# Kernel optimization log

Hardware: AMD Instinct MI355X
Metric: run time of the kernel (lower is better)

The kernel has to match this reference:

```python
import jax, jax.numpy as jnp
import numpy as np

EPS = 1e-5  # torch BatchNorm1d default eps


def _bn(x, gamma, beta):
    # Training-mode BatchNorm1d: per-batch mean/var (biased), affine.
    mu = jnp.mean(x, axis=0)
    var = jnp.var(x, axis=0)
    return (x - mu) * jax.lax.rsqrt(var + EPS) * gamma + beta


def _trunk(x, layers):
    # For each hidden layer: Tanh(Linear(BatchNorm(x)))
    for (W, b, g, be) in layers:
        x = jnp.tanh(_bn(x, g, be) @ W + b)
    return x


def setup_inputs() -> dict:
    key = jax.random.key(0)
    ks = jax.random.split(key, 16)
    B, N, D = 4096, 8192, 1024
    dims = [D, 1024, 512, 256]
    inp = {
        "x": jax.random.normal(ks[0], (B, D), dtype=jnp.float32),
        "x_n": jax.random.normal(ks[1], (N, D), dtype=jnp.float32),
        "y_n": jax.random.uniform(ks[2], (N, 1), dtype=jnp.float32),
    }
    for i in range(3):
        fan_in, fan_out = dims[i], dims[i + 1]
        bound = 1.0 / np.sqrt(fan_in)
        inp[f"W{i+1}"] = jax.random.uniform(ks[3 + 4 * i], (fan_in, fan_out), minval=-bound, maxval=bound, dtype=jnp.float32)
        inp[f"b{i+1}"] = jax.random.uniform(ks[4 + 4 * i], (fan_out,), minval=-bound, maxval=bound, dtype=jnp.float32)
        inp[f"g{i+1}"] = jnp.ones((fan_in,), dtype=jnp.float32)
        inp[f"beta{i+1}"] = jnp.zeros((fan_in,), dtype=jnp.float32)
    return inp


def reference(x, x_n, y_n,
              W1, b1, g1, beta1,
              W2, b2, g2, beta2,
              W3, b3, g3, beta3):
    layers = [(W1, b1, g1, beta1), (W2, b2, g2, beta2), (W3, b3, g3, beta3)]
    q = _trunk(x, layers)      # [B, 256]
    k = _trunk(x_n, layers)    # [N, 256]
    # l2 similarity: negative squared euclidean distance, via GEMM.
    # sim[i,j] = -||q_i - k_j||^2 = 2 q_i.k_j - ||q_i||^2 - ||k_j||^2
    q2 = jnp.sum(q * q, axis=1, keepdims=True)          # [B,1]
    k2 = jnp.sum(k * k, axis=1)                          # [N]
    sim = 2.0 * (q @ k.T) - q2 - k2[None, :]             # [B,N]
    # x != x_n (different shapes) => train=False, no diagonal masking.
    scores = jax.nn.softmax(sim, axis=1)
    out = jnp.clip(scores @ y_n, 0.0, 1.0)               # [B,1]
    return jnp.squeeze(out, axis=1)                      # [B]
```

## Files before the change

### kernel.cpp

```cpp
#include <hip/hip_runtime.h>
#include <math.h>
#include <stdint.h>


typedef __attribute__((ext_vector_type(8))) _Float16 half8;
typedef __attribute__((ext_vector_type(4))) _Float16 half4;
typedef __attribute__((ext_vector_type(4))) float floatx4;

__device__ __forceinline__ float fast_tanh(float x) {
    float ax = fabsf(x);
    float e  = __expf(-2.0f * ax);
    float r  = (1.0f - e) / (1.0f + e);
    return copysignf(r, x);
}
__device__ __forceinline__ void gload16(const void* g, void* l) {
    __builtin_amdgcn_global_load_lds(
        (__attribute__((address_space(1))) void*)(uintptr_t)(g),
        (__attribute__((address_space(3))) void*)(unsigned int)(uintptr_t)(l),
        16, 0, 0);
}

__global__ __launch_bounds__(256) void tof16_stats_all(
        const float* __restrict__ xn, const float* __restrict__ x,
        _Float16* __restrict__ xnh, _Float16* __restrict__ xh,
        float* __restrict__ cs0, float* __restrict__ cq0,
        float* __restrict__ cs3, float* __restrict__ cq3) {
    const float* in; _Float16* out; float *cs, *cq; int r0;
    if (blockIdx.x < 256) { in = xn; out = xnh; cs = cs0; cq = cq0; r0 = blockIdx.x * 32; }
    else                  { in = x;  out = xh;  cs = cs3; cq = cq3; r0 = (blockIdx.x - 256) * 32; }
    const int c = threadIdx.x * 4;
    float s0 = 0.f, s1 = 0.f, s2 = 0.f, s3 = 0.f;
    float q0 = 0.f, q1 = 0.f, q2 = 0.f, q3 = 0.f;
    for (int r = r0; r < r0 + 32; ++r) {
        float4 v = *(const float4*)&in[(size_t)r * 1024 + c];
        half4 h;
        h[0] = (_Float16)v.x; h[1] = (_Float16)v.y;
        h[2] = (_Float16)v.z; h[3] = (_Float16)v.w;
        *(half4*)&out[(size_t)r * 1024 + c] = h;
        s0 += v.x; q0 += v.x * v.x;
        s1 += v.y; q1 += v.y * v.y;
        s2 += v.z; q2 += v.z * v.z;
        s3 += v.w; q3 += v.w * v.w;
    }
    atomicAdd(&cs[c + 0], s0); atomicAdd(&cq[c + 0], q0);
    atomicAdd(&cs[c + 1], s1); atomicAdd(&cq[c + 1], q1);
    atomicAdd(&cs[c + 2], s2); atomicAdd(&cq[c + 2], q2);
    atomicAdd(&cs[c + 3], s3); atomicAdd(&cq[c + 3], q3);
}

__global__ __launch_bounds__(256) void wprep2(
        const float* __restrict__ W, const float* __restrict__ g,
        const float* __restrict__ beta,
        const float* __restrict__ csK, const float* __restrict__ cqK, float invRK,
        _Float16* __restrict__ WTk, float* __restrict__ baccK,
        const float* __restrict__ csQ, const float* __restrict__ cqQ, float invRQ,
        _Float16* __restrict__ WTq, float* __restrict__ baccQ,
        int C, int F) {
    const int z = blockIdx.z;
    const float* cs = z ? csQ : csK;
    const float* cq = z ? cqQ : cqK;
    const float invR = z ? invRQ : invRK;
    _Float16* WT = z ? WTq : WTk;
    float* bacc = z ? baccQ : baccK;

    __shared__ float sv[32], tv[32];
    __shared__ float tile[32][33];
    __shared__ float lds2[8][32];
    const int c0 = blockIdx.y * 32, f0 = blockIdx.x * 32;
    const int tx = threadIdx.x & 31, ty = threadIdx.x >> 5;
    if (ty == 0) {
        int c = c0 + tx;
        float mean = cs[c] * invR;
        float var  = fmaxf(cq[c] * invR - mean * mean, 0.f);
        float s    = g[c] * rsqrtf(var + 1e-5f);
        sv[tx] = s;
        tv[tx] = beta[c] - mean * s;
    }
    __syncthreads();
    float pacc = 0.f;
#pragma unroll
    for (int i = 0; i < 32; i += 8) {
        float w = W[(size_t)(c0 + ty + i) * F + f0 + tx];
        tile[ty + i][tx] = w * sv[ty + i];
        pacc += w * tv[ty + i];
    }
    lds2[ty][tx] = pacc;
    __syncthreads();
#pragma unroll
    for (int i = 0; i < 32; i += 8)
        WT[(size_t)(f0 + ty + i) * C + c0 + tx] = (_Float16)tile[tx][ty + i];
    if (ty == 0) {
        float a = 0.f;
#pragma unroll
        for (int j = 0; j < 8; ++j) a += lds2[j][tx];
        atomicAdd(&bacc[f0 + tx], a);
    }
}

__global__ __launch_bounds__(256, 2) void gemm_tn_tanh(
        const _Float16* __restrict__ Ak, const _Float16* __restrict__ Aq,
        const _Float16* __restrict__ WTk, const _Float16* __restrict__ WTq,
        const float* __restrict__ bias,
        const float* __restrict__ baccK, const float* __restrict__ baccQ,
        _Float16* __restrict__ Yk, _Float16* __restrict__ Yq,
        int K, int F, int smodeK, int smodeQ,
        float* __restrict__ csK, float* __restrict__ cqK,
        float* __restrict__ csQ, float* __restrict__ cqQ,
        float* __restrict__ rowsqK) {
    __shared__ _Float16 As[128 * 64];
    __shared__ _Float16 Bs[128 * 64];
    const int tid = threadIdx.x;
    const int wv = tid >> 6, ln = tid & 63;
    const int quad = ln >> 4, l16 = ln & 15;
    const int wr = wv >> 1, wc = wv & 1;

    const bool isK = blockIdx.x < 64;
    const _Float16* A  = isK ? Ak : Aq;
    const _Float16* WT = isK ? WTk : WTq;
    const float* bacc  = isK ? baccK : baccQ;
    _Float16* Y        = isK ? Yk : Yq;
    const int smode    = isK ? smodeK : smodeQ;
    float* cs = isK ? csK : csQ;
    float* cq = isK ? cqK : cqQ;
    const int i0 = (isK ? blockIdx.x : blockIdx.x - 64) * 128;
    const int f0 = blockIdx.y * 128;

    floatx4 acc[4][4];
#pragma unroll
    for (int a = 0; a < 4; ++a)
#pragma unroll
        for (int b = 0; b < 4; ++b) acc[a][b] = (floatx4)0.f;

    for (int k0 = 0; k0 < K; k0 += 64) {
        const char* Ab = (const char*)(A + (size_t)i0 * K + k0);
        const char* Bb = (const char*)(WT + (size_t)f0 * K + k0);
#pragma unroll
        for (int it = 0; it < 4; ++it) {
            int seg = it * 256 + tid;
            int row = seg >> 3, p = seg & 7;
            int lcol = (p ^ row) & 7;
            gload16(Ab + (size_t)row * (K * 2) + lcol * 16, (char*)As + seg * 16);
        }
#pragma unroll
        for (int it = 0; it < 4; ++it) {
            int seg = it * 256 + tid;
            int row = seg >> 3, p = seg & 7;
            int lcol = (p ^ row) & 7;
            gload16(Bb + (size_t)row * (K * 2) + lcol * 16, (char*)Bs + seg * 16);
        }
        __syncthreads();
#pragma unroll
        for (int kk = 0; kk < 2; ++kk) {
            half8 af[4], bf[4];
#pragma unroll
            for (int t = 0; t < 4; ++t) {
                int ra = wr * 64 + t * 16 + l16;
                int ca = ((kk * 4 + quad) ^ ra) & 7;
                af[t] = *(const half8*)((const char*)As + ra * 128 + ca * 16);
                int rb = wc * 64 + t * 16 + l16;
                int cb = ((kk * 4 + quad) ^ rb) & 7;
                bf[t] = *(const half8*)((const char*)Bs + rb * 128 + cb * 16);
            }
#pragma unroll
            for (int tr = 0; tr < 4; ++tr)
#pragma unroll
                for (int tc = 0; tc < 4; ++tc)
                    acc[tr][tc] = __builtin_amdgcn_mfma_f32_16x16x32_f16(af[tr], bf[tc], acc[tr][tc], 0, 0, 0);
        }
        __syncthreads();
    }
#pragma unroll
    for (int tc = 0; tc < 4; ++tc) {
        int f = f0 + wc * 64 + tc * 16 + l16;
        float bb = bias[f] + bacc[f];
#pragma unroll
        for (int tr = 0; tr < 4; ++tr)
#pragma unroll
            for (int r = 0; r < 4; ++r) {
                int row = i0 + wr * 64 + tr * 16 + quad * 4 + r;
                float v = fast_tanh(acc[tr][tc][r] + bb);
                acc[tr][tc][r] = v;
                Y[(size_t)row * F + f] = (_Float16)v;
            }
    }
    if (smode == 1) {
#pragma unroll
        for (int tc = 0; tc < 4; ++tc) {
            int f = f0 + wc * 64 + tc * 16 + l16;
            float s = 0.f, q = 0.f;
#pragma unroll
            for (int tr = 0; tr < 4; ++tr)
#pragma unroll
                for (int r = 0; r < 4; ++r) {
                    float v = acc[tr][tc][r];
                    s += v; q += v * v;
                }
            s += __shfl_xor(s, 16); q += __shfl_xor(q, 16);
            s += __shfl_xor(s, 32); q += __shfl_xor(q, 32);
            if (quad == 0) {
                atomicAdd(&cs[f], s);
                atomicAdd(&cq[f], q);
            }
        }
    } else if (smode == 2) {
#pragma unroll
        for (int tr = 0; tr < 4; ++tr)
#pragma unroll
            for (int r = 0; r < 4; ++r) {
                float rq = 0.f;
#pragma unroll
                for (int tc = 0; tc < 4; ++tc) {
                    float v = acc[tr][tc][r];
                    rq += v * v;
                }
                rq += __shfl_xor(rq, 1); rq += __shfl_xor(rq, 2);
                rq += __shfl_xor(rq, 4); rq += __shfl_xor(rq, 8);
                if (l16 == 0)
                    atomicAdd(&rowsqK[i0 + wr * 64 + tr * 16 + quad * 4 + r], rq);
            }
    }
}

__global__ __launch_bounds__(256, 2) void flash_mfma(
        const _Float16* __restrict__ Q, const _Float16* __restrict__ K3,
        const float* __restrict__ k2n, const float* __restrict__ yv,
        float* __restrict__ pm, float* __restrict__ pl, float* __restrict__ po,
        int jlen, int nsplit) {
    __shared__ _Float16 Ts[128 * 256];
    const int tid = threadIdx.x;
    const int wv = tid >> 6, ln = tid & 63;
    const int quad = ln >> 4, l16 = ln & 15;
    const int i0 = blockIdx.x * 128;
    const int jb = blockIdx.y * jlen;
    const int nch = jlen >> 7;

    auto stageTile = [&](const _Float16* src, int row0) {
        const char* sb = (const char*)(src + (size_t)row0 * 256);
#pragma unroll
        for (int it = 0; it < 16; ++it) {
            int seg = it * 256 + tid;
            int row = seg >> 5, p = seg & 31;
            int lcol = (p & 24) | ((p ^ row) & 7);
            gload16(sb + (size_t)row * 512 + lcol * 16, (char*)Ts + seg * 16);
        }
    };

    stageTile(Q, i0);
    __syncthreads();
    half8 qf[2][8];
#pragma unroll
    for (int tr = 0; tr < 2; ++tr)
#pragma unroll
        for (int k0 = 0; k0 < 8; ++k0) {
            int row = wv * 32 + tr * 16 + l16;
            int c = k0 * 4 + quad;
            int phys = (c & 24) | ((c ^ row) & 7);
            qf[tr][k0] = *(const half8*)((const char*)Ts + row * 512 + phys * 16);
        }
    asm volatile("s_waitcnt lgkmcnt(0)" ::: "memory");
    __syncthreads();

    float mrun[2][4], lrun[2][4], orun[2][4];
#pragma unroll
    for (int tr = 0; tr < 2; ++tr)
#pragma unroll
        for (int r = 0; r < 4; ++r) { mrun[tr][r] = -INFINITY; lrun[tr][r] = 0.f; orun[tr][r] = 0.f; }

    stageTile(K3, jb);
    __syncthreads();
    for (int jc = 0; jc < nch; ++jc) {
        const int j0 = jb + jc * 128;
        floatx4 acc[2][8];
#pragma unroll
        for (int a = 0; a < 2; ++a)
#pragma unroll
            for (int b = 0; b < 8; ++b) acc[a][b] = (floatx4)0.f;
#pragma unroll
        for (int k0 = 0; k0 < 8; ++k0) {
            half8 kf[8];
#pragma unroll
            for (int tc = 0; tc < 8; ++tc) {
                int row = tc * 16 + l16;
                int c = k0 * 4 + quad;
                int phys = (c & 24) | ((c ^ row) & 7);
                kf[tc] = *(const half8*)((const char*)Ts + row * 512 + phys * 16);
            }
#pragma unroll
            for (int tr = 0; tr < 2; ++tr)
#pragma unroll
                for (int tc = 0; tc < 8; ++tc)
                    acc[tr][tc] = __builtin_amdgcn_mfma_f32_16x16x32_f16(qf[tr][k0], kf[tc], acc[tr][tc], 0, 0, 0);
        }
        __syncthreads();
        if (jc + 1 < nch) stageTile(K3, j0 + 128);
        float k2v[8], yv8[8];
#pragma unroll
        for (int tc = 0; tc < 8; ++tc) {
            int j = j0 + tc * 16 + l16;
            k2v[tc] = k2n[j];
            yv8[tc] = yv[j];
        }
#pragma unroll
        for (int tr = 0; tr < 2; ++tr)
#pragma unroll
            for (int r = 0; r < 4; ++r) {
                float lg[8], mt = -INFINITY;
#pragma unroll
                for (int tc = 0; tc < 8; ++tc) {
                    lg[tc] = 2.f * acc[tr][tc][r] - k2v[tc];
                    mt = fmaxf(mt, lg[tc]);
                }
#pragma unroll
                for (int m = 1; m < 16; m <<= 1) mt = fmaxf(mt, __shfl_xor(mt, m));
                float mnew = fmaxf(mrun[tr][r], mt);
                float sp = 0.f, spy = 0.f;
#pragma unroll
                for (int tc = 0; tc < 8; ++tc) {
                    float p = __expf(lg[tc] - mnew);
                    sp  += p;
                    spy += p * yv8[tc];
                }
#pragma unroll
                for (int m = 1; m < 16; m <<= 1) {
                    sp  += __shfl_xor(sp, m);
                    spy += __shfl_xor(spy, m);
                }
                float sc = __expf(mrun[tr][r] - mnew);
                lrun[tr][r] = lrun[tr][r] * sc + sp;
                orun[tr][r] = orun[tr][r] * sc + spy;
                mrun[tr][r] = mnew;
            }
        if (jc + 1 < nch) __syncthreads();
    }
    if (l16 == 0) {
#pragma unroll
        for (int tr = 0; tr < 2; ++tr)
#pragma unroll
            for (int r = 0; r < 4; ++r) {
                int row = i0 + wv * 32 + tr * 16 + quad * 4 + r;
                size_t idx = (size_t)row * nsplit + blockIdx.y;
                pm[idx] = mrun[tr][r];
                pl[idx] = lrun[tr][r];
                po[idx] = orun[tr][r];
            }
    }
}

__global__ void combine_k(const float* __restrict__ pm, const float* __restrict__ pl,
                          const float* __restrict__ po, float* __restrict__ out,
                          int B, int nsplit) {
    int i = blockIdx.x * blockDim.x + threadIdx.x;
    if (i >= B) return;
    float M = -INFINITY;
    for (int s = 0; s < nsplit; ++s) M = fmaxf(M, pm[(size_t)i * nsplit + s]);
    float L = 0.f, O = 0.f;
    for (int s = 0; s < nsplit; ++s) {
        float w = __expf(pm[(size_t)i * nsplit + s] - M);
        L += pl[(size_t)i * nsplit + s] * w;
        O += po[(size_t)i * nsplit + s] * w;
    }
    float r = O / L;
    out[i] = fminf(fmaxf(r, 0.f), 1.f);
}

extern "C" void kernel_launch(void* const* d_in, const int* in_sizes, int n_in,
                              void* d_out, int out_size, void* d_ws, size_t ws_size,
                              hipStream_t stream) {
    const float* x   = (const float*)d_in[0];
    const float* x_n = (const float*)d_in[1];
    const float* y_n = (const float*)d_in[2];
    const float* Wm[3]    = {(const float*)d_in[3],  (const float*)d_in[7],  (const float*)d_in[11]};
    const float* bm[3]    = {(const float*)d_in[4],  (const float*)d_in[8],  (const float*)d_in[12]};
    const float* gm[3]    = {(const float*)d_in[5],  (const float*)d_in[9],  (const float*)d_in[13]};
    const float* betam[3] = {(const float*)d_in[6],  (const float*)d_in[10], (const float*)d_in[14]};
    (void)in_sizes; (void)n_in; (void)out_size; (void)ws_size;

    const int B = 4096, N = 8192;
    const int NSPLIT = 16;
    const size_t M1 = 1024 * 1024;

    _Float16* h0 = (_Float16*)d_ws;
    _Float16* h1 = h0 + 8 * M1;
    _Float16* h2 = h1 + 4 * M1;
    _Float16* h3 = h2 + 8 * M1;
    _Float16* WTk = h3 + 4 * M1;
    _Float16* WTq = WTk + M1;
    float* fb = (float*)(WTq + M1);
    float* csA[6], *cqA[6];
    for (int i = 0; i < 6; ++i) { csA[i] = fb + i * 2048; cqA[i] = fb + i * 2048 + 1024; }
    float* baccK[3], *baccQ[3];
    for (int i = 0; i < 3; ++i) { baccK[i] = fb + 12288 + i * 1024; baccQ[i] = fb + 15360 + i * 1024; }
    float* k2n = fb + 18432;
    const size_t zero_floats = 18432 + 8192;
    float* pm = fb + zero_floats;
    float* pl = pm + (size_t)B * NSPLIT;
    float* po = pl + (size_t)B * NSPLIT;

    _Float16* xnh = h0, *xh = h1;
    _Float16* actAk = h2, *actAq = h3;
    _Float16* actBk = h0, *actBq = h1;
    _Float16* k3 = h2, *q3 = h2 + 2 * M1;

    hipMemsetAsync(fb, 0, zero_floats * sizeof(float), stream);
    tof16_stats_all<<<384, 256, 0, stream>>>(x_n, x, xnh, xh,
                                             csA[0], cqA[0], csA[3], cqA[3]);
    const float invRK = 1.0f / (float)N, invRQ = 1.0f / (float)B;

    wprep2<<<dim3(1024 / 32, 1024 / 32, 2), 256, 0, stream>>>(
        Wm[0], gm[0], betam[0], csA[0], cqA[0], invRK, WTk, baccK[0],
        csA[3], cqA[3], invRQ, WTq, baccQ[0], 1024, 1024);
    gemm_tn_tanh<<<dim3(96, 1024 / 128), 256, 0, stream>>>(
        xnh, xh, WTk, WTq, bm[0], baccK[0], baccQ[0], actAk, actAq,
        1024, 1024, 1, 1, csA[1], cqA[1], csA[4], cqA[4], nullptr);
    wprep2<<<dim3(512 / 32, 1024 / 32, 2), 256, 0, stream>>>(
        Wm[1], gm[1], betam[1], csA[1], cqA[1], invRK, WTk, baccK[1],
        csA[4], cqA[4], invRQ, WTq, baccQ[1], 1024, 512);
    gemm_tn_tanh<<<dim3(96, 512 / 128), 256, 0, stream>>>(
        actAk, actAq, WTk, WTq, bm[1], baccK[1], baccQ[1], actBk, actBq,
        1024, 512, 1, 1, csA[2], cqA[2], csA[5], cqA[5], nullptr);
    wprep2<<<dim3(256 / 32, 512 / 32, 2), 256, 0, stream>>>(
        Wm[2], gm[2], betam[2], csA[2], cqA[2], invRK, WTk, baccK[2],
        csA[5], cqA[5], invRQ, WTq, baccQ[2], 512, 256);
    gemm_tn_tanh<<<dim3(96, 256 / 128), 256, 0, stream>>>(
        actBk, actBq, WTk, WTq, bm[2], baccK[2], baccQ[2], k3, q3,
        512, 256, 2, 0, nullptr, nullptr, nullptr, nullptr, k2n);

    flash_mfma<<<dim3(B / 128, NSPLIT), 256, 0, stream>>>(
        q3, k3, k2n, y_n, pm, pl, po, N / NSPLIT, NSPLIT);
    combine_k<<<B / 256, 256, 0, stream>>>(pm, pl, po, (float*)d_out, B, NSPLIT);
}
```

Baseline: 281.4 us.

## Shrink flash tile to 64 keys, defer cross-lane softmax reduction, use exp2 domain

The flash softmax kernel now stages 64-row K tiles, halving LDS and accumulator registers, and raises launch bounds to 4 blocks per CU with twice as many key splits. Each lane keeps its own running max/sum per row and merges across the 16 lanes only once at the end, replacing per-chunk shuffle reductions. Logits are pre-scaled into the base-2 domain (k2 scaled by log2 e in the stats kernel, dot product scaled by 2·log2 e) so exp2f is used throughout. This trades less Q-fragment reuse per tile and more partials to combine for higher occupancy and fewer shuffles.

```diff
diff --git a/kernel.cpp b/kernel.cpp
--- a/kernel.cpp
+++ b/kernel.cpp
@@ -6,6 +6,9 @@
 typedef __attribute__((ext_vector_type(8))) _Float16 half8;
 typedef __attribute__((ext_vector_type(4))) _Float16 half4;
 typedef __attribute__((ext_vector_type(4))) float floatx4;
+
+#define L2E  1.4426950408889634f
+#define SCALE2 2.8853901817f
 
 __device__ __forceinline__ float fast_tanh(float x) {
     float ax = fabsf(x);
@@ -216,28 +219,28 @@
                 rq += __shfl_xor(rq, 1); rq += __shfl_xor(rq, 2);
                 rq += __shfl_xor(rq, 4); rq += __shfl_xor(rq, 8);
                 if (l16 == 0)
-                    atomicAdd(&rowsqK[i0 + wr * 64 + tr * 16 + quad * 4 + r], rq);
-            }
-    }
-}
-
-__global__ __launch_bounds__(256, 2) void flash_mfma(
+                    atomicAdd(&rowsqK[i0 + wr * 64 + tr * 16 + quad * 4 + r], rq * L2E);
+            }
+    }
+}
+
+__global__ __launch_bounds__(256, 4) void flash_mfma(
         const _Float16* __restrict__ Q, const _Float16* __restrict__ K3,
-        const float* __restrict__ k2n, const float* __restrict__ yv,
+        const float* __restrict__ k2s, const float* __restrict__ yv,
         float* __restrict__ pm, float* __restrict__ pl, float* __restrict__ po,
         int jlen, int nsplit) {
-    __shared__ _Float16 Ts[128 * 256];
+    __shared__ _Float16 Ts[64 * 256];
     const int tid = threadIdx.x;
     const int wv = tid >> 6, ln = tid & 63;
     const int quad = ln >> 4, l16 = ln & 15;
     const int i0 = blockIdx.x * 128;
     const int jb = blockIdx.y * jlen;
-    const int nch = jlen >> 7;
-
-    auto stageTile = [&](const _Float16* src, int row0) {
-        const char* sb = (const char*)(src + (size_t)row0 * 256);
-#pragma unroll
-        for (int it = 0; it < 16; ++it) {
+    const int nch = jlen >> 6;
+
+    auto stage64 = [&](const _Float16* src) {
+        const char* sb = (const char*)src;
+#pragma unroll
+        for (int it = 0; it < 8; ++it) {
             int seg = it * 256 + tid;
             int row = seg >> 5, p = seg & 31;
             int lcol = (p & 24) | ((p ^ row) & 7);
@@ -245,41 +248,46 @@
         }
     };
 
-    stageTile(Q, i0);
-    __syncthreads();
     half8 qf[2][8];
 #pragma unroll
+    for (int h = 0; h < 2; ++h) {
+        stage64(Q + (size_t)(i0 + h * 64) * 256);
+        __syncthreads();
+        if ((wv >> 1) == h) {
+#pragma unroll
+            for (int tr = 0; tr < 2; ++tr)
+#pragma unroll
+                for (int k0 = 0; k0 < 8; ++k0) {
+                    int row = (wv & 1) * 32 + tr * 16 + l16;
+                    int c = k0 * 4 + quad;
+                    int phys = (c & 24) | ((c ^ row) & 7);
+                    qf[tr][k0] = *(const half8*)((const char*)Ts + row * 512 + phys * 16);
+                }
+            asm volatile("s_waitcnt lgkmcnt(0)" ::: "memory");
+        }
+        __syncthreads();
+    }
+
+    float mrun[2][4], lrun[2][4], orun[2][4];
+#pragma unroll
     for (int tr = 0; tr < 2; ++tr)
 #pragma unroll
-        for (int k0 = 0; k0 < 8; ++k0) {
-            int row = wv * 32 + tr * 16 + l16;
-            int c = k0 * 4 + quad;
-            int phys = (c & 24) | ((c ^ row) & 7);
-            qf[tr][k0] = *(const half8*)((const char*)Ts + row * 512 + phys * 16);
-        }
-    asm volatile("s_waitcnt lgkmcnt(0)" ::: "memory");
-    __syncthreads();
-
-    float mrun[2][4], lrun[2][4], orun[2][4];
-#pragma unroll
-    for (int tr = 0; tr < 2; ++tr)
-#pragma unroll
         for (int r = 0; r < 4; ++r) { mrun[tr][r] = -INFINITY; lrun[tr][r] = 0.f; orun[tr][r] = 0.f; }
 
-    stageTile(K3, jb);
+    stage64(K3 + (size_t)jb * 256);
     __syncthreads();
     for (int jc = 0; jc < nch; ++jc) {
-        const int j0 = jb + jc * 128;
-        floatx4 acc[2][8];
+        const int j0 = jb + jc * 64;
+        floatx4 acc[2][4];
 #pragma unroll
         for (int a = 0; a < 2; ++a)
 #pragma unroll
-            for (int b = 0; b < 8; ++b) acc[a][b] = (floatx4)0.f;
+            for (int b = 0; b < 4; ++b) acc[a][b] = (floatx4)0.f;
 #pragma unroll
         for (int k0 = 0; k0 < 8; ++k0) {
-            half8 kf[8];
-#pragma unroll
-            for (int tc = 0; tc < 8; ++tc) {
+            half8 kf[4];
+#pragma unroll
+            for (int tc = 0; tc < 4; ++tc) {
                 int row = tc * 16 + l16;
                 int c = k0 * 4 + quad;
                 int phys = (c & 24) | ((c ^ row) & 7);
@@ -288,62 +296,67 @@
 #pragma unroll
             for (int tr = 0; tr < 2; ++tr)
 #pragma unroll
-                for (int tc = 0; tc < 8; ++tc)
+                for (int tc = 0; tc < 4; ++tc)
                     acc[tr][tc] = __builtin_amdgcn_mfma_f32_16x16x32_f16(qf[tr][k0], kf[tc], acc[tr][tc], 0, 0, 0);
         }
         __syncthreads();
-        if (jc + 1 < nch) stageTile(K3, j0 + 128);
-        float k2v[8], yv8[8];
-#pragma unroll
-        for (int tc = 0; tc < 8; ++tc) {
+        if (jc + 1 < nch) stage64(K3 + (size_t)(j0 + 64) * 256);
+        float k2v[4], yv4[4];
+#pragma unroll
+        for (int tc = 0; tc < 4; ++tc) {
             int j = j0 + tc * 16 + l16;
-            k2v[tc] = k2n[j];
-            yv8[tc] = yv[j];
+            k2v[tc] = k2s[j];
+            yv4[tc] = yv[j];
         }
 #pragma unroll
         for (int tr = 0; tr < 2; ++tr)
 #pragma unroll
             for (int r = 0; r < 4; ++r) {
-                float lg[8], mt = -INFINITY;
-#pragma unroll
-                for (int tc = 0; tc < 8; ++tc) {
-                    lg[tc] = 2.f * acc[tr][tc][r] - k2v[tc];
+                float lg[4], mt = -INFINITY;
+#pragma unroll
+                for (int tc = 0; tc < 4; ++tc) {
+                    lg[tc] = SCALE2 * acc[tr][tc][r] - k2v[tc];
                     mt = fmaxf(mt, lg[tc]);
                 }
-#pragma unroll
-                for (int m = 1; m < 16; m <<= 1) mt = fmaxf(mt, __shfl_xor(mt, m));
                 float mnew = fmaxf(mrun[tr][r], mt);
+                float sc = exp2f(mrun[tr][r] - mnew);
                 float sp = 0.f, spy = 0.f;
 #pragma unroll
-                for (int tc = 0; tc < 8; ++tc) {
-                    float p = __expf(lg[tc] - mnew);
+                for (int tc = 0; tc < 4; ++tc) {
+                    float p = exp2f(lg[tc] - mnew);
                     sp  += p;
-                    spy += p * yv8[tc];
+                    spy += p * yv4[tc];
                 }
-#pragma unroll
-                for (int m = 1; m < 16; m <<= 1) {
-                    sp  += __shfl_xor(sp, m);
-                    spy += __shfl_xor(spy, m);
-                }
-                float sc = __expf(mrun[tr][r] - mnew);
                 lrun[tr][r] = lrun[tr][r] * sc + sp;
                 orun[tr][r] = orun[tr][r] * sc + spy;
                 mrun[tr][r] = mnew;
             }
         if (jc + 1 < nch) __syncthreads();
     }
-    if (l16 == 0) {
-#pragma unroll
-        for (int tr = 0; tr < 2; ++tr)
-#pragma unroll
-            for (int r = 0; r < 4; ++r) {
+#pragma unroll
+    for (int tr = 0; tr < 2; ++tr)
+#pragma unroll
+        for (int r = 0; r < 4; ++r) {
+            float m = mrun[tr][r], l = lrun[tr][r], o = orun[tr][r];
+#pragma unroll
+            for (int s = 1; s < 16; s <<= 1) {
+                float m2 = __shfl_xor(m, s);
+                float l2 = __shfl_xor(l, s);
+                float o2 = __shfl_xor(o, s);
+                float mn = fmaxf(m, m2);
+                float a = exp2f(m - mn), b = exp2f(m2 - mn);
+                l = l * a + l2 * b;
+                o = o * a + o2 * b;
+                m = mn;
+            }
+            if (l16 == 0) {
                 int row = i0 + wv * 32 + tr * 16 + quad * 4 + r;
                 size_t idx = (size_t)row * nsplit + blockIdx.y;
-                pm[idx] = mrun[tr][r];
-                pl[idx] = lrun[tr][r];
-                po[idx] = orun[tr][r];
-            }
-    }
+                pm[idx] = m;
+                pl[idx] = l;
+                po[idx] = o;
+            }
+        }
 }
 
 __global__ void combine_k(const float* __restrict__ pm, const float* __restrict__ pl,
@@ -355,7 +368,7 @@
     for (int s = 0; s < nsplit; ++s) M = fmaxf(M, pm[(size_t)i * nsplit + s]);
     float L = 0.f, O = 0.f;
     for (int s = 0; s < nsplit; ++s) {
-        float w = __expf(pm[(size_t)i * nsplit + s] - M);
+        float w = exp2f(pm[(size_t)i * nsplit + s] - M);
         L += pl[(size_t)i * nsplit + s] * w;
         O += po[(size_t)i * nsplit + s] * w;
     }
@@ -376,7 +389,7 @@
     (void)in_sizes; (void)n_in; (void)out_size; (void)ws_size;
 
     const int B = 4096, N = 8192;
-    const int NSPLIT = 16;
+    const int NSPLIT = 32;
     const size_t M1 = 1024 * 1024;
 
     _Float16* h0 = (_Float16*)d_ws;
```

Result: slower. 326.4 us (+16.0%).
